# Performance work log

Measured on AMD Instinct MI355X. Metric: run time of the kernel, lower is better.

The kernel has to match this reference:

```python
import jax, jax.numpy as jnp
import numpy as np

EMBED_DIM = 1024
NUM_HEADS = 16
HEAD_DIM = EMBED_DIM // NUM_HEADS


def setup_inputs() -> dict:
    key = jax.random.key(0)
    ks = jax.random.split(key, 6)
    B, S, D = 4, 2048, EMBED_DIM
    std = 1.0 / np.sqrt(D)
    x = jax.random.normal(ks[0], (B, S, D), dtype=jnp.float32)
    wq = jax.random.normal(ks[1], (D, D), dtype=jnp.float32) * std
    wk = jax.random.normal(ks[2], (D, D), dtype=jnp.float32) * std
    wv = jax.random.normal(ks[3], (D, D), dtype=jnp.float32) * std
    wo = jax.random.normal(ks[4], (D, D), dtype=jnp.float32) * std
    bo = jax.random.normal(ks[5], (D,), dtype=jnp.float32) * 0.01
    return {"x": x, "wq": wq, "wk": wk, "wv": wv, "wo": wo, "bo": bo}


def reference(x, wq, wk, wv, wo, bo):
    B, S, D = x.shape
    H, Hd = NUM_HEADS, HEAD_DIM
    scale = 1.0 / jnp.sqrt(jnp.asarray(Hd, x.dtype))
    # nn.Linear computes x @ W.T; split into heads -> [B, H, S, Hd]
    q = (x @ wq.T).reshape(B, S, H, Hd).transpose(0, 2, 1, 3)
    k = (x @ wk.T).reshape(B, S, H, Hd).transpose(0, 2, 1, 3)
    v = (x @ wv.T).reshape(B, S, H, Hd).transpose(0, 2, 1, 3)
    scores = jnp.einsum("bhqd,bhkd->bhqk", q, k) * scale  # [B,H,S,S]
    attn = jax.nn.softmax(scores, axis=-1)
    ctx = jnp.einsum("bhqk,bhkd->bhqd", attn, v)
    ctx = ctx.transpose(0, 2, 1, 3).reshape(B, S, D)
    return ctx @ wo.T + bo
```

## Files before the change

kernel.cpp:

```cpp
#include <hip/hip_runtime.h>

typedef __bf16 bf16x8 __attribute__((ext_vector_type(8)));
typedef float f32x4 __attribute__((ext_vector_type(4)));
typedef unsigned u32x4 __attribute__((ext_vector_type(4)));
typedef unsigned short u16;

#define GAS __attribute__((address_space(1)))
#define LAS __attribute__((address_space(3)))

static __device__ __forceinline__ void gload16(const void* g, void* l) {
  __builtin_amdgcn_global_load_lds((const GAS unsigned int*)g, (LAS unsigned int*)l, 16, 0, 0);
}

static __device__ __forceinline__ u16 f2bf(float f) {
  unsigned u = __builtin_bit_cast(unsigned, f);
  u += 0x7fffu + ((u >> 16) & 1u);
  return (u16)(u >> 16);
}

static __device__ __forceinline__ unsigned pk2(float lo, float hi) {
  ushort2 u;
  u.x = __builtin_bit_cast(u16, (__bf16)lo);
  u.y = __builtin_bit_cast(u16, (__bf16)hi);
  return __builtin_bit_cast(unsigned, u);
}

static __device__ __forceinline__ f32x4 vmax4(f32x4 a, f32x4 b) {
  f32x4 r;
  r[0] = fmaxf(a[0], b[0]); r[1] = fmaxf(a[1], b[1]);
  r[2] = fmaxf(a[2], b[2]); r[3] = fmaxf(a[3], b[3]);
  return r;
}

__global__ void cvt_kernel(const float* __restrict__ src, u16* __restrict__ dst, int n4) {
  int i = blockIdx.x * 256 + threadIdx.x;
  if (i >= n4) return;
  float4 v = reinterpret_cast<const float4*>(src)[i];
  ushort4 o;
  o.x = f2bf(v.x); o.y = f2bf(v.y); o.z = f2bf(v.z); o.w = f2bf(v.w);
  reinterpret_cast<ushort4*>(dst)[i] = o;
}

__global__ void cvt_w_kernel(const float* __restrict__ w0, const float* __restrict__ w1,
                             const float* __restrict__ w2, const float* __restrict__ w3,
                             u16* __restrict__ d0, u16* __restrict__ d1,
                             u16* __restrict__ d2, u16* __restrict__ d3) {
  int sel = blockIdx.x >> 10;
  int i = (blockIdx.x & 1023) * 256 + threadIdx.x;
  const float* s = sel == 0 ? w0 : sel == 1 ? w1 : sel == 2 ? w2 : w3;
  u16* d = sel == 0 ? d0 : sel == 1 ? d1 : sel == 2 ? d2 : d3;
  float4 v = reinterpret_cast<const float4*>(s)[i];
  ushort4 o;
  o.x = f2bf(v.x); o.y = f2bf(v.y); o.z = f2bf(v.z); o.w = f2bf(v.w);
  reinterpret_cast<ushort4*>(d)[i] = o;
}

__global__ void gemm_qkv(const u16* __restrict__ A, const u16* __restrict__ W,
                         u16* __restrict__ Qo, u16* __restrict__ Ko, u16* __restrict__ Vo) {
  __shared__ u16 As[128 * 32];
  __shared__ u16 Bs[128 * 32];
  const int t = threadIdx.x;
  const int lane = t & 63;
  const int w = t >> 6;
  const int wr = w >> 1, wc = w & 1;
  const int l15 = lane & 15, lhi = lane >> 4;
  const int swz = (blockIdx.x & 7) * 192 + (blockIdx.x >> 3);
  const int bm = swz / 24, bn = swz % 24;

  f32x4 acc[4][4];
#pragma unroll
  for (int a = 0; a < 4; ++a)
#pragma unroll
    for (int b = 0; b < 4; ++b) acc[a][b] = (f32x4){0.f, 0.f, 0.f, 0.f};

  const u16* ag = A + (size_t)(bm * 128 + (t >> 2)) * 1024 + (t & 3) * 8;
  const u16* bg = W + (size_t)(bn * 128 + (t >> 2)) * 1024 + (t & 3) * 8;
  u16* as_p = &As[t * 8];
  u16* bs_p = &Bs[t * 8];

  for (int kt = 0; kt < 32; ++kt) {
    gload16(ag, as_p);
    gload16(ag + 64 * 1024, as_p + 2048);
    gload16(bg, bs_p);
    gload16(bg + 64 * 1024, bs_p + 2048);
    ag += 32; bg += 32;
    __syncthreads();
    bf16x8 af[4], bfr[4];
#pragma unroll
    for (int mt = 0; mt < 4; ++mt)
      af[mt] = *(const bf16x8*)&As[(wr * 64 + mt * 16 + l15) * 32 + lhi * 8];
#pragma unroll
    for (int nt = 0; nt < 4; ++nt)
      bfr[nt] = *(const bf16x8*)&Bs[(wc * 64 + nt * 16 + l15) * 32 + lhi * 8];
#pragma unroll
    for (int mt = 0; mt < 4; ++mt)
#pragma unroll
      for (int nt = 0; nt < 4; ++nt)
        acc[mt][nt] = __builtin_amdgcn_mfma_f32_16x16x32_bf16(af[mt], bfr[nt], acc[mt][nt], 0, 0, 0);
    __syncthreads();
  }

  const int tsel = bn >> 3;
  const int m0 = bm * 128 + wr * 64;
  const int n0 = bn * 128 + wc * 64;
  const int bb = bm >> 4;
  if (tsel == 0) {
    const float qs = 0.125f * 1.4426950408889634f;
#pragma unroll
    for (int nt = 0; nt < 4; ++nt) {
      int n = n0 + nt * 16 + l15;
      int c = n & 1023, h = c >> 6, hd = c & 63;
      size_t base = (size_t)(bb * 16 + h) * 2048 * 64 + hd;
#pragma unroll
      for (int mt = 0; mt < 4; ++mt)
#pragma unroll
        for (int i = 0; i < 4; ++i) {
          int s = (m0 + mt * 16 + lhi * 4 + i) & 2047;
          Qo[base + (size_t)s * 64] = f2bf(acc[mt][nt][i] * qs);
        }
    }
  } else if (tsel == 1) {
#pragma unroll
    for (int nt = 0; nt < 4; ++nt) {
      int n = n0 + nt * 16 + l15;
      int c = n & 1023, h = c >> 6, hd = c & 63;
      size_t base = (size_t)(bb * 16 + h) * 2048 * 64 + hd;
#pragma unroll
      for (int mt = 0; mt < 4; ++mt)
#pragma unroll
        for (int i = 0; i < 4; ++i) {
          int s = (m0 + mt * 16 + lhi * 4 + i) & 2047;
          Ko[base + (size_t)s * 64] = f2bf(acc[mt][nt][i]);
        }
    }
  } else {
#pragma unroll
    for (int nt = 0; nt < 4; ++nt) {
      int n = n0 + nt * 16 + l15;
      int c = n & 1023, h = c >> 6, hd = c & 63;
#pragma unroll
      for (int mt = 0; mt < 4; ++mt) {
        int s0 = (m0 + mt * 16 + lhi * 4) & 2047;
        int sp0 = ((s0 >> 4) & 1) * 4 + ((s0 >> 2) & 3) * 8 + (s0 >> 5) * 32;
        ushort4 pk;
        pk.x = f2bf(acc[mt][nt][0]);
        pk.y = f2bf(acc[mt][nt][1]);
        pk.z = f2bf(acc[mt][nt][2]);
        pk.w = f2bf(acc[mt][nt][3]);
        *(ushort4*)&Vo[((size_t)(bb * 16 + h) * 64 + hd) * 2048 + sp0] = pk;
      }
    }
  }
}

__global__ __launch_bounds__(256, 4) void attn_kernel(const u16* __restrict__ Q,
                                                      const u16* __restrict__ K,
                                                      const u16* __restrict__ Vp,
                                                      u16* __restrict__ Ctx) {
  __shared__ u16 Ks[2 * 64 * 64];
  __shared__ u16 Vs[2 * 64 * 64];
  const int t = threadIdx.x;
  const int lane = t & 63;
  const int w = t >> 6;
  const int l15 = lane & 15, lhi = lane >> 4;
  const int swz = (blockIdx.x & 7) * 128 + (blockIdx.x >> 3);
  const int qt = swz & 15, pair = swz >> 4;
  const u16* qp = Q + (size_t)pair * 2048 * 64;
  const u16* kp = K + (size_t)pair * 2048 * 64;
  const u16* vp = Vp + (size_t)pair * 64 * 2048;

  const int qrA = qt * 128 + w * 32 + l15;
  bf16x8 qfA[2], qfB[2];
  qfA[0] = *(const bf16x8*)&qp[(size_t)qrA * 64 + lhi * 8];
  qfA[1] = *(const bf16x8*)&qp[(size_t)qrA * 64 + 32 + lhi * 8];
  qfB[0] = *(const bf16x8*)&qp[(size_t)(qrA + 16) * 64 + lhi * 8];
  qfB[1] = *(const bf16x8*)&qp[(size_t)(qrA + 16) * 64 + 32 + lhi * 8];

  const u32x4 ow = {0x3F803F80u, 0x3F803F80u, 0x3F803F80u, 0x3F803F80u};
  const bf16x8 onesf = __builtin_bit_cast(bf16x8, ow);

  const int swzq = (l15 & 7) << 3;
  const int kofs0 = l15 * 64 + ((lhi * 8) ^ swzq);
  const int kofs1 = l15 * 64 + ((32 + lhi * 8) ^ swzq);

  float mA = -1e30f, mB = -1e30f;
  f32x4 coA[4], coB[4], laA, laB;
  laA = (f32x4){0.f, 0.f, 0.f, 0.f};
  laB = laA;
#pragma unroll
  for (int n = 0; n < 4; ++n) { coA[n] = laA; coB[n] = laA; }

  auto stage = [&](int cb, int tt) {
#pragma unroll
    for (int j = 0; j < 2; ++j) {
      int c = j * 256 + t;
      int r = c >> 3, c8 = (c & 7) * 8;
      gload16(kp + (size_t)(tt * 64 + r) * 64 + (c8 ^ ((r & 7) << 3)), &Ks[cb + c * 8]);
    }
#pragma unroll
    for (int j = 0; j < 2; ++j) {
      int c = j * 256 + t;
      int r = c >> 3, c8 = (c & 7) * 8;
      gload16(vp + (size_t)r * 2048 + tt * 64 + (c8 ^ ((r & 7) << 3)), &Vs[cb + c * 8]);
    }
  };

  auto softmax_sub = [&](f32x4 (&sa)[4], float& m, f32x4 (&co)[4], f32x4& lacc,
                         unsigned (&pw)[4][2]) {
    f32x4 t0 = vmax4(vmax4(sa[0], sa[1]), vmax4(sa[2], sa[3]));
    float mx = fmaxf(fmaxf(t0[0], t0[1]), fmaxf(t0[2], t0[3]));
    mx = fmaxf(mx, __shfl_xor(mx, 16));
    mx = fmaxf(mx, __shfl_xor(mx, 32));
    if (!__all(mx - m <= 8.0f)) {
      float mn = fmaxf(m, mx);
      float sc = __builtin_exp2f(m - mn);
      float si0 = __shfl(sc, lhi * 4 + 0);
      float si1 = __shfl(sc, lhi * 4 + 1);
      float si2 = __shfl(sc, lhi * 4 + 2);
      float si3 = __shfl(sc, lhi * 4 + 3);
      lacc[0] *= si0; lacc[1] *= si1; lacc[2] *= si2; lacc[3] *= si3;
#pragma unroll
      for (int nthd = 0; nthd < 4; ++nthd) {
        co[nthd][0] *= si0; co[nthd][1] *= si1;
        co[nthd][2] *= si2; co[nthd][3] *= si3;
      }
      m = mn;
    }
#pragma unroll
    for (int nt = 0; nt < 4; ++nt)
#pragma unroll
      for (int e = 0; e < 4; ++e) sa[nt][e] = __builtin_exp2f(sa[nt][e] - m);
#pragma unroll
    for (int nt = 0; nt < 4; ++nt) {
      pw[nt][0] = pk2(sa[nt][0], sa[nt][1]);
      pw[nt][1] = pk2(sa[nt][2], sa[nt][3]);
    }
  };

  stage(0, 0);

  for (int kt = 0; kt < 32; ++kt) {
    const int cb = (kt & 1) * 4096;
    if (kt < 31) {
      stage(cb ^ 4096, kt + 1);
      asm volatile("s_waitcnt vmcnt(4)" ::: "memory");
    } else {
      asm volatile("s_waitcnt vmcnt(0)" ::: "memory");
    }
    __builtin_amdgcn_s_barrier();

    f32x4 saA[4], saB[4];
    __builtin_amdgcn_s_setprio(1);
#pragma unroll
    for (int nt = 0; nt < 4; ++nt) {
      saA[nt] = (f32x4){0.f, 0.f, 0.f, 0.f};
      saB[nt] = saA[nt];
      bf16x8 kf0 = *(const bf16x8*)&Ks[cb + kofs0 + nt * 1024];
      bf16x8 kf1 = *(const bf16x8*)&Ks[cb + kofs1 + nt * 1024];
      saA[nt] = __builtin_amdgcn_mfma_f32_16x16x32_bf16(kf0, qfA[0], saA[nt], 0, 0, 0);
      saB[nt] = __builtin_amdgcn_mfma_f32_16x16x32_bf16(kf0, qfB[0], saB[nt], 0, 0, 0);
      saA[nt] = __builtin_amdgcn_mfma_f32_16x16x32_bf16(kf1, qfA[1], saA[nt], 0, 0, 0);
      saB[nt] = __builtin_amdgcn_mfma_f32_16x16x32_bf16(kf1, qfB[1], saB[nt], 0, 0, 0);
    }
    __builtin_amdgcn_s_setprio(0);

    unsigned pwA[4][2], pwB[4][2];
    softmax_sub(saA, mA, coA, laA, pwA);
    softmax_sub(saB, mB, coB, laB, pwB);

    __builtin_amdgcn_s_setprio(1);
#pragma unroll
    for (int ks = 0; ks < 2; ++ks) {
      u32x4 awA = {pwA[2 * ks][0], pwA[2 * ks][1], pwA[2 * ks + 1][0], pwA[2 * ks + 1][1]};
      u32x4 awB = {pwB[2 * ks][0], pwB[2 * ks][1], pwB[2 * ks + 1][0], pwB[2 * ks + 1][1]};
      bf16x8 afA = __builtin_bit_cast(bf16x8, awA);
      bf16x8 afB = __builtin_bit_cast(bf16x8, awB);
      laA = __builtin_amdgcn_mfma_f32_16x16x32_bf16(afA, onesf, laA, 0, 0, 0);
      laB = __builtin_amdgcn_mfma_f32_16x16x32_bf16(afB, onesf, laB, 0, 0, 0);
      const int vo = l15 * 64 + (((ks ? 32 : 0) + lhi * 8) ^ swzq);
#pragma unroll
      for (int nthd = 0; nthd < 4; ++nthd) {
        bf16x8 vf = *(const bf16x8*)&Vs[cb + vo + nthd * 1024];
        coA[nthd] = __builtin_amdgcn_mfma_f32_16x16x32_bf16(afA, vf, coA[nthd], 0, 0, 0);
        coB[nthd] = __builtin_amdgcn_mfma_f32_16x16x32_bf16(afB, vf, coB[nthd], 0, 0, 0);
      }
    }
    __builtin_amdgcn_s_setprio(0);
    __builtin_amdgcn_s_barrier();
  }

  float liA[4], liB[4];
#pragma unroll
  for (int i = 0; i < 4; ++i) {
    liA[i] = 1.0f / laA[i];
    liB[i] = 1.0f / laB[i];
  }
  const int bb = pair >> 4, hh = pair & 15;
  const int sbase = qt * 128 + w * 32 + lhi * 4;
#pragma unroll
  for (int nthd = 0; nthd < 4; ++nthd) {
    int hd = nthd * 16 + l15;
#pragma unroll
    for (int i = 0; i < 4; ++i) {
      Ctx[(size_t)(bb * 2048 + sbase + i) * 1024 + hh * 64 + hd] = f2bf(coA[nthd][i] * liA[i]);
      Ctx[(size_t)(bb * 2048 + sbase + 16 + i) * 1024 + hh * 64 + hd] = f2bf(coB[nthd][i] * liB[i]);
    }
  }
}

__global__ void gemm_out(const u16* __restrict__ A, const u16* __restrict__ W,
                         const float* __restrict__ Bo, float* __restrict__ Out) {
  __shared__ u16 As[128 * 32];
  __shared__ u16 Bs[128 * 32];
  const int t = threadIdx.x;
  const int lane = t & 63;
  const int w = t >> 6;
  const int wr = w >> 1, wc = w & 1;
  const int l15 = lane & 15, lhi = lane >> 4;
  const int swz = (blockIdx.x & 7) * 64 + (blockIdx.x >> 3);
  const int bm = swz >> 3, bn = swz & 7;

  f32x4 acc[4][4];
#pragma unroll
  for (int a = 0; a < 4; ++a)
#pragma unroll
    for (int b = 0; b < 4; ++b) acc[a][b] = (f32x4){0.f, 0.f, 0.f, 0.f};

  const u16* ag = A + (size_t)(bm * 128 + (t >> 2)) * 1024 + (t & 3) * 8;
  const u16* bg = W + (size_t)(bn * 128 + (t >> 2)) * 1024 + (t & 3) * 8;
  u16* as_p = &As[t * 8];
  u16* bs_p = &Bs[t * 8];

  for (int kt = 0; kt < 32; ++kt) {
    gload16(ag, as_p);
    gload16(ag + 64 * 1024, as_p + 2048);
    gload16(bg, bs_p);
    gload16(bg + 64 * 1024, bs_p + 2048);
    ag += 32; bg += 32;
    __syncthreads();
    bf16x8 af[4], bfr[4];
#pragma unroll
    for (int mt = 0; mt < 4; ++mt)
      af[mt] = *(const bf16x8*)&As[(wr * 64 + mt * 16 + l15) * 32 + lhi * 8];
#pragma unroll
    for (int nt = 0; nt < 4; ++nt)
      bfr[nt] = *(const bf16x8*)&Bs[(wc * 64 + nt * 16 + l15) * 32 + lhi * 8];
#pragma unroll
    for (int mt = 0; mt < 4; ++mt)
#pragma unroll
      for (int nt = 0; nt < 4; ++nt)
        acc[mt][nt] = __builtin_amdgcn_mfma_f32_16x16x32_bf16(af[mt], bfr[nt], acc[mt][nt], 0, 0, 0);
    __syncthreads();
  }

  const int m0 = bm * 128 + wr * 64;
  const int n0 = bn * 128 + wc * 64;
#pragma unroll
  for (int nt = 0; nt < 4; ++nt) {
    int n = n0 + nt * 16 + l15;
    float bias = Bo[n];
#pragma unroll
    for (int mt = 0; mt < 4; ++mt)
#pragma unroll
      for (int i = 0; i < 4; ++i) {
        int m = m0 + mt * 16 + lhi * 4 + i;
        Out[(size_t)m * 1024 + n] = acc[mt][nt][i] + bias;
      }
  }
}

extern "C" void kernel_launch(void* const* d_in, const int* in_sizes, int n_in,
                              void* d_out, int out_size, void* d_ws, size_t ws_size,
                              hipStream_t stream) {
  const float* x  = (const float*)d_in[0];
  const float* wq = (const float*)d_in[1];
  const float* wk = (const float*)d_in[2];
  const float* wv = (const float*)d_in[3];
  const float* wo = (const float*)d_in[4];
  const float* bo = (const float*)d_in[5];
  float* out = (float*)d_out;

  u16* xb    = (u16*)d_ws;
  u16* wqkvb = xb + (size_t)8 * 1024 * 1024;
  u16* wob   = wqkvb + (size_t)3 * 1024 * 1024;
  u16* qb    = wob + (size_t)1 * 1024 * 1024;
  u16* kb    = qb + (size_t)8 * 1024 * 1024;
  u16* vtb   = kb + (size_t)8 * 1024 * 1024;
  u16* ctxb  = xb;

  cvt_kernel<<<8192, 256, 0, stream>>>(x, xb, 2097152);
  cvt_w_kernel<<<4096, 256, 0, stream>>>(wq, wk, wv, wo,
                                         wqkvb, wqkvb + 1048576, wqkvb + 2097152, wob);
  gemm_qkv<<<64 * 24, 256, 0, stream>>>(xb, wqkvb, qb, kb, vtb);
  attn_kernel<<<1024, 256, 0, stream>>>(qb, kb, vtb, ctxb);
  gemm_out<<<64 * 8, 256, 0, stream>>>(ctxb, wob, bo, out);
}
```

Baseline: 234.3 us.

## Double query tile per attention block to reuse K/V tiles across more rows

```diff
diff --git a/kernel.cpp b/kernel.cpp
--- a/kernel.cpp
+++ b/kernel.cpp
@@ -153,7 +153,7 @@
   }
 }
 
-__global__ __launch_bounds__(256, 4) void attn_kernel(const u16* __restrict__ Q,
+__global__ __launch_bounds__(256, 2) void attn_kernel(const u16* __restrict__ Q,
                                                       const u16* __restrict__ K,
                                                       const u16* __restrict__ Vp,
                                                       u16* __restrict__ Ctx) {
@@ -163,18 +163,19 @@
   const int lane = t & 63;
   const int w = t >> 6;
   const int l15 = lane & 15, lhi = lane >> 4;
-  const int swz = (blockIdx.x & 7) * 128 + (blockIdx.x >> 3);
-  const int qt = swz & 15, pair = swz >> 4;
+  const int swz = (blockIdx.x & 7) * 64 + (blockIdx.x >> 3);
+  const int qt = swz & 7, pair = swz >> 3;
   const u16* qp = Q + (size_t)pair * 2048 * 64;
   const u16* kp = K + (size_t)pair * 2048 * 64;
   const u16* vp = Vp + (size_t)pair * 64 * 2048;
 
-  const int qrA = qt * 128 + w * 32 + l15;
-  bf16x8 qfA[2], qfB[2];
-  qfA[0] = *(const bf16x8*)&qp[(size_t)qrA * 64 + lhi * 8];
-  qfA[1] = *(const bf16x8*)&qp[(size_t)qrA * 64 + 32 + lhi * 8];
-  qfB[0] = *(const bf16x8*)&qp[(size_t)(qrA + 16) * 64 + lhi * 8];
-  qfB[1] = *(const bf16x8*)&qp[(size_t)(qrA + 16) * 64 + 32 + lhi * 8];
+  const int qr0 = qt * 256 + w * 64 + l15;
+  bf16x8 qf[4][2];
+#pragma unroll
+  for (int s = 0; s < 4; ++s) {
+    qf[s][0] = *(const bf16x8*)&qp[(size_t)(qr0 + s * 16) * 64 + lhi * 8];
+    qf[s][1] = *(const bf16x8*)&qp[(size_t)(qr0 + s * 16) * 64 + 32 + lhi * 8];
+  }
 
   const u32x4 ow = {0x3F803F80u, 0x3F803F80u, 0x3F803F80u, 0x3F803F80u};
   const bf16x8 onesf = __builtin_bit_cast(bf16x8, ow);
@@ -183,12 +184,14 @@
   const int kofs0 = l15 * 64 + ((lhi * 8) ^ swzq);
   const int kofs1 = l15 * 64 + ((32 + lhi * 8) ^ swzq);
 
-  float mA = -1e30f, mB = -1e30f;
-  f32x4 coA[4], coB[4], laA, laB;
-  laA = (f32x4){0.f, 0.f, 0.f, 0.f};
-  laB = laA;
-#pragma unroll
-  for (int n = 0; n < 4; ++n) { coA[n] = laA; coB[n] = laA; }
+  float m[4] = {-1e30f, -1e30f, -1e30f, -1e30f};
+  f32x4 co[4][4], la[4];
+#pragma unroll
+  for (int s = 0; s < 4; ++s) {
+    la[s] = (f32x4){0.f, 0.f, 0.f, 0.f};
+#pragma unroll
+    for (int n = 0; n < 4; ++n) co[s][n] = la[s];
+  }
 
   auto stage = [&](int cb, int tt) {
 #pragma unroll
@@ -205,15 +208,15 @@
     }
   };
 
-  auto softmax_sub = [&](f32x4 (&sa)[4], float& m, f32x4 (&co)[4], f32x4& lacc,
+  auto softmax_sub = [&](f32x4 (&sa)[4], float& mm, f32x4 (&co_)[4], f32x4& lacc,
                          unsigned (&pw)[4][2]) {
     f32x4 t0 = vmax4(vmax4(sa[0], sa[1]), vmax4(sa[2], sa[3]));
-    float mx = fmaxf(fmaxf(t0[0], t0[1]), fmaxf(t0[2], t0[3]));
-    mx = fmaxf(mx, __shfl_xor(mx, 16));
-    mx = fmaxf(mx, __shfl_xor(mx, 32));
-    if (!__all(mx - m <= 8.0f)) {
-      float mn = fmaxf(m, mx);
-      float sc = __builtin_exp2f(m - mn);
+    float mxl = fmaxf(fmaxf(t0[0], t0[1]), fmaxf(t0[2], t0[3]));
+    if (!__all(mxl - mm <= 8.0f)) {
+      float mx = fmaxf(mxl, __shfl_xor(mxl, 16));
+      mx = fmaxf(mx, __shfl_xor(mx, 32));
+      float mn = fmaxf(mm, mx);
+      float sc = __builtin_exp2f(mm - mn);
       float si0 = __shfl(sc, lhi * 4 + 0);
       float si1 = __shfl(sc, lhi * 4 + 1);
       float si2 = __shfl(sc, lhi * 4 + 2);
@@ -221,15 +224,15 @@
       lacc[0] *= si0; lacc[1] *= si1; lacc[2] *= si2; lacc[3] *= si3;
 #pragma unroll
       for (int nthd = 0; nthd < 4; ++nthd) {
-        co[nthd][0] *= si0; co[nthd][1] *= si1;
-        co[nthd][2] *= si2; co[nthd][3] *= si3;
+        co_[nthd][0] *= si0; co_[nthd][1] *= si1;
+        co_[nthd][2] *= si2; co_[nthd][3] *= si3;
       }
-      m = mn;
+      mm = mn;
     }
 #pragma unroll
     for (int nt = 0; nt < 4; ++nt)
 #pragma unroll
-      for (int e = 0; e < 4; ++e) sa[nt][e] = __builtin_exp2f(sa[nt][e] - m);
+      for (int e = 0; e < 4; ++e) sa[nt][e] = __builtin_exp2f(sa[nt][e] - mm);
 #pragma unroll
     for (int nt = 0; nt < 4; ++nt) {
       pw[nt][0] = pk2(sa[nt][0], sa[nt][1]);
@@ -249,61 +252,61 @@
     }
     __builtin_amdgcn_s_barrier();
 
-    f32x4 saA[4], saB[4];
+    f32x4 sa[4][4];
     __builtin_amdgcn_s_setprio(1);
 #pragma unroll
     for (int nt = 0; nt < 4; ++nt) {
-      saA[nt] = (f32x4){0.f, 0.f, 0.f, 0.f};
-      saB[nt] = saA[nt];
       bf16x8 kf0 = *(const bf16x8*)&Ks[cb + kofs0 + nt * 1024];
       bf16x8 kf1 = *(const bf16x8*)&Ks[cb + kofs1 + nt * 1024];
-      saA[nt] = __builtin_amdgcn_mfma_f32_16x16x32_bf16(kf0, qfA[0], saA[nt], 0, 0, 0);
-      saB[nt] = __builtin_amdgcn_mfma_f32_16x16x32_bf16(kf0, qfB[0], saB[nt], 0, 0, 0);
-      saA[nt] = __builtin_amdgcn_mfma_f32_16x16x32_bf16(kf1, qfA[1], saA[nt], 0, 0, 0);
-      saB[nt] = __builtin_amdgcn_mfma_f32_16x16x32_bf16(kf1, qfB[1], saB[nt], 0, 0, 0);
+#pragma unroll
+      for (int s = 0; s < 4; ++s) {
+        f32x4 z = (f32x4){0.f, 0.f, 0.f, 0.f};
+        z = __builtin_amdgcn_mfma_f32_16x16x32_bf16(kf0, qf[s][0], z, 0, 0, 0);
+        sa[s][nt] = __builtin_amdgcn_mfma_f32_16x16x32_bf16(kf1, qf[s][1], z, 0, 0, 0);
+      }
     }
     __builtin_amdgcn_s_setprio(0);
 
-    unsigned pwA[4][2], pwB[4][2];
-    softmax_sub(saA, mA, coA, laA, pwA);
-    softmax_sub(saB, mB, coB, laB, pwB);
+    unsigned pw[4][4][2];
+#pragma unroll
+    for (int s = 0; s < 4; ++s) softmax_sub(sa[s], m[s], co[s], la[s], pw[s]);
 
     __builtin_amdgcn_s_setprio(1);
 #pragma unroll
     for (int ks = 0; ks < 2; ++ks) {
-      u32x4 awA = {pwA[2 * ks][0], pwA[2 * ks][1], pwA[2 * ks + 1][0], pwA[2 * ks + 1][1]};
-      u32x4 awB = {pwB[2 * ks][0], pwB[2 * ks][1], pwB[2 * ks + 1][0], pwB[2 * ks + 1][1]};
-      bf16x8 afA = __builtin_bit_cast(bf16x8, awA);
-      bf16x8 afB = __builtin_bit_cast(bf16x8, awB);
-      laA = __builtin_amdgcn_mfma_f32_16x16x32_bf16(afA, onesf, laA, 0, 0, 0);
-      laB = __builtin_amdgcn_mfma_f32_16x16x32_bf16(afB, onesf, laB, 0, 0, 0);
       const int vo = l15 * 64 + (((ks ? 32 : 0) + lhi * 8) ^ swzq);
-#pragma unroll
-      for (int nthd = 0; nthd < 4; ++nthd) {
-        bf16x8 vf = *(const bf16x8*)&Vs[cb + vo + nthd * 1024];
-        coA[nthd] = __builtin_amdgcn_mfma_f32_16x16x32_bf16(afA, vf, coA[nthd], 0, 0, 0);
-        coB[nthd] = __builtin_amdgcn_mfma_f32_16x16x32_bf16(afB, vf, coB[nthd], 0, 0, 0);
+      bf16x8 vf[4];
+#pragma unroll
+      for (int nthd = 0; nthd < 4; ++nthd)
+        vf[nthd] = *(const bf16x8*)&Vs[cb + vo + nthd * 1024];
+#pragma unroll
+      for (int s = 0; s < 4; ++s) {
+        u32x4 aw = {pw[s][2 * ks][0], pw[s][2 * ks][1], pw[s][2 * ks + 1][0], pw[s][2 * ks + 1][1]};
+        bf16x8 af = __builtin_bit_cast(bf16x8, aw);
+        la[s] = __builtin_amdgcn_mfma_f32_16x16x32_bf16(af, onesf, la[s], 0, 0, 0);
+#pragma unroll
+        for (int nthd = 0; nthd < 4; ++nthd)
+          co[s][nthd] = __builtin_amdgcn_mfma_f32_16x16x32_bf16(af, vf[nthd], co[s][nthd], 0, 0, 0);
       }
     }
     __builtin_amdgcn_s_setprio(0);
     __builtin_amdgcn_s_barrier();
   }
 
-  float liA[4], liB[4];
-#pragma unroll
-  for (int i = 0; i < 4; ++i) {
-    liA[i] = 1.0f / laA[i];
-    liB[i] = 1.0f / laB[i];
-  }
   const int bb = pair >> 4, hh = pair & 15;
-  const int sbase = qt * 128 + w * 32 + lhi * 4;
-#pragma unroll
-  for (int nthd = 0; nthd < 4; ++nthd) {
-    int hd = nthd * 16 + l15;
-#pragma unroll
-    for (int i = 0; i < 4; ++i) {
-      Ctx[(size_t)(bb * 2048 + sbase + i) * 1024 + hh * 64 + hd] = f2bf(coA[nthd][i] * liA[i]);
-      Ctx[(size_t)(bb * 2048 + sbase + 16 + i) * 1024 + hh * 64 + hd] = f2bf(coB[nthd][i] * liB[i]);
+  const int sbase = qt * 256 + w * 64 + lhi * 4;
+#pragma unroll
+  for (int s = 0; s < 4; ++s) {
+    float li[4];
+#pragma unroll
+    for (int i = 0; i < 4; ++i) li[i] = 1.0f / la[s][i];
+#pragma unroll
+    for (int nthd = 0; nthd < 4; ++nthd) {
+      int hd = nthd * 16 + l15;
+#pragma unroll
+      for (int i = 0; i < 4; ++i)
+        Ctx[(size_t)(bb * 2048 + sbase + s * 16 + i) * 1024 + hh * 64 + hd] =
+            f2bf(co[s][nthd][i] * li[i]);
     }
   }
 }
@@ -392,6 +395,6 @@
   cvt_w_kernel<<<4096, 256, 0, stream>>>(wq, wk, wv, wo,
                                          wqkvb, wqkvb + 1048576, wqkvb + 2097152, wob);
   gemm_qkv<<<64 * 24, 256, 0, stream>>>(xb, wqkvb, qb, kb, vtb);
-  attn_kernel<<<1024, 256, 0, stream>>>(qb, kb, vtb, ctxb);
+  attn_kernel<<<512, 256, 0, stream>>>(qb, kb, vtb, ctxb);
   gemm_out<<<64 * 8, 256, 0, stream>>>(ctxb, wob, bo, out);
 }
```

After: 232.5 us. No clear change (-0.7%).
